# Performance work log

Hardware: AMD Instinct MI355X
Metric: run time of the kernel (lower is better)

Reference implementation:

```python
import jax, jax.numpy as jnp
import numpy as np
import math

NUM_PARAM = 9
STRIDE = 1
BN_EPS = 1e-5


def _make_p_n(N):
    # matches LDConv._get_p_n: irregular kernel offset grid of N points
    base = round(math.sqrt(N))
    rows = N // base
    mod = N % base
    gx, gy = np.meshgrid(np.arange(rows), np.arange(base), indexing='ij')
    px, py = gx.ravel(), gy.ravel()
    if mod > 0:
        mx, my = np.meshgrid(np.arange(rows, rows + 1), np.arange(mod), indexing='ij')
        px = np.concatenate([px, mx.ravel()])
        py = np.concatenate([py, my.ravel()])
    return jnp.asarray(np.concatenate([px, py]), jnp.float32).reshape(1, 2 * N, 1, 1)


def _conv2d_same(x, w, stride, pad):
    return jax.lax.conv_general_dilated(
        x, w, (stride, stride), [(pad, pad), (pad, pad)],
        dimension_numbers=('NCHW', 'OIHW', 'NCHW'))


def _gather(xf, q, W, N):
    # xf: (b,c,H*W); q: (b,h,w,2N) int indices -> (b,c,h,w,N)
    idx = q[..., :N] * W + q[..., N:]
    return jax.vmap(lambda xb, ib: xb[:, ib])(xf, idx)


def setup_inputs() -> dict:
    key = jax.random.key(0)
    ks = jax.random.split(key, 3)
    B, C, H, W = 8, 128, 64, 64
    outc = 256
    x = jax.random.normal(ks[0], (B, C, H, W), jnp.float32)
    # p_conv init: uniform(-1e-4, 1e-4) weights, zero bias (per the torch module)
    p_conv_w = jax.random.uniform(ks[1], (2 * NUM_PARAM, C, 3, 3), jnp.float32, -1e-4, 1e-4)
    p_conv_b = jnp.zeros((2 * NUM_PARAM,), jnp.float32)
    conv_w = jax.random.normal(ks[2], (outc, C, NUM_PARAM, 1), jnp.float32) / math.sqrt(C * NUM_PARAM)
    bn_gamma = jnp.ones((outc,), jnp.float32)
    bn_beta = jnp.zeros((outc,), jnp.float32)
    bn_mean = jnp.zeros((outc,), jnp.float32)
    bn_var = jnp.ones((outc,), jnp.float32)
    return dict(x=x, p_conv_w=p_conv_w, p_conv_b=p_conv_b, conv_w=conv_w,
                bn_gamma=bn_gamma, bn_beta=bn_beta, bn_mean=bn_mean, bn_var=bn_var)


def reference(x, p_conv_w, p_conv_b, conv_w, bn_gamma, bn_beta, bn_mean, bn_var):
    N = NUM_PARAM
    B, C, H, W = x.shape
    offset = _conv2d_same(x, p_conv_w, STRIDE, 1) + p_conv_b[None, :, None, None]  # (b,2N,h,w)
    h, w = offset.shape[2], offset.shape[3]
    gx, gy = jnp.meshgrid(jnp.arange(0, h * STRIDE, STRIDE),
                          jnp.arange(0, w * STRIDE, STRIDE), indexing='ij')
    p_0 = jnp.concatenate([jnp.broadcast_to(gx, (1, N, h, w)),
                           jnp.broadcast_to(gy, (1, N, h, w))], axis=1).astype(x.dtype)
    p = (p_0 + _make_p_n(N) + offset).transpose(0, 2, 3, 1)  # (b,h,w,2N)

    q_lt = jnp.floor(jax.lax.stop_gradient(p))
    q_rb = q_lt + 1
    clampi = lambda q: jnp.concatenate([jnp.clip(q[..., :N], 0, H - 1),
                                        jnp.clip(q[..., N:], 0, W - 1)], -1).astype(jnp.int32)
    q_lt = clampi(q_lt)
    q_rb = clampi(q_rb)
    q_lb = jnp.concatenate([q_lt[..., :N], q_rb[..., N:]], -1)
    q_rt = jnp.concatenate([q_rb[..., :N], q_lt[..., N:]], -1)
    p = jnp.concatenate([jnp.clip(p[..., :N], 0, H - 1),
                         jnp.clip(p[..., N:], 0, W - 1)], -1)
    f = lambda q: q.astype(p.dtype)
    g_lt = (1 + (f(q_lt[..., :N]) - p[..., :N])) * (1 + (f(q_lt[..., N:]) - p[..., N:]))
    g_rb = (1 - (f(q_rb[..., :N]) - p[..., :N])) * (1 - (f(q_rb[..., N:]) - p[..., N:]))
    g_lb = (1 + (f(q_lb[..., :N]) - p[..., :N])) * (1 - (f(q_lb[..., N:]) - p[..., N:]))
    g_rt = (1 - (f(q_rt[..., :N]) - p[..., :N])) * (1 + (f(q_rt[..., N:]) - p[..., N:]))

    xf = x.reshape(B, C, H * W)
    x_off = (g_lt[:, None] * _gather(xf, q_lt, W, N)
             + g_rb[:, None] * _gather(xf, q_rb, W, N)
             + g_lb[:, None] * _gather(xf, q_lb, W, N)
             + g_rt[:, None] * _gather(xf, q_rt, W, N))  # (b,c,h,w,N)
    # rearrange 'b c h w n -> b c (h n) w'
    x_off = x_off.transpose(0, 1, 2, 4, 3).reshape(B, C, h * N, w)

    y = jax.lax.conv_general_dilated(x_off, conv_w, (N, 1), 'VALID',
                                     dimension_numbers=('NCHW', 'OIHW', 'NCHW'))
    scale = (bn_gamma / jnp.sqrt(bn_var + BN_EPS))[None, :, None, None]
    y = (y - bn_mean[None, :, None, None]) * scale + bn_beta[None, :, None, None]
    return y * jax.nn.sigmoid(y)  # SiLU
```

## Files before the change

### kernel.cpp

```cpp
#include <hip/hip_runtime.h>
#include <hip/hip_bf16.h>
#include <cstdint>

#define B_   8
#define C_   128
#define H_   64
#define W_   64
#define NPT  9
#define OC   256
#define K_   (C_*NPT)
#define HW   (H_*W_)
#define XTPB 557568

typedef __attribute__((ext_vector_type(8))) short short8;
typedef __attribute__((ext_vector_type(4))) float f32x4;
typedef __attribute__((ext_vector_type(4))) unsigned int u32x4;

static __device__ __forceinline__ unsigned short f2bf(float f) {
    union { float f; unsigned u; } a; a.f = f;
    unsigned r = a.u + 0x7fffu + ((a.u >> 16) & 1u);
    return (unsigned short)(r >> 16);
}
static __device__ __forceinline__ float bf2f(unsigned short u) {
    union { unsigned u; float f; } a; a.u = ((unsigned)u) << 16;
    return a.f;
}

__global__ __launch_bounds__(256) void k_transpose2(const float* __restrict__ x,
                                                    unsigned short* __restrict__ xh,
                                                    unsigned short* __restrict__ xl) {
    __shared__ float sp[128][65];
    int b = blockIdx.x >> 6, i = blockIdx.x & 63;
    int t = threadIdx.x;
    const float* xb = x + (size_t)b * C_ * HW + i * 64;
#pragma unroll
    for (int it = 0; it < 8; ++it) {
        int q = it * 256 + t;
        int c = q >> 4, j4 = q & 15;
        *(f32x4*)&sp[c][j4 * 4] = *(const f32x4*)(xb + (size_t)c * HW + j4 * 4);
    }
    __syncthreads();
    size_t obase = (size_t)b * XTPB + ((size_t)(i + 1) * 66 + 1) * 128;
#pragma unroll
    for (int it = 0; it < 4; ++it) {
        int q = it * 256 + t;
        int j = q >> 4, cg = q & 15;
        u32x4 ph, pl;
#pragma unroll
        for (int p2 = 0; p2 < 4; ++p2) {
            float a = sp[cg * 8 + p2 * 2][j];
            float bb = sp[cg * 8 + p2 * 2 + 1][j];
            unsigned short ah = f2bf(a), bh = f2bf(bb);
            unsigned short al = f2bf(a - bf2f(ah)), bl = f2bf(bb - bf2f(bh));
            ph[p2] = (uint32_t)ah | ((uint32_t)bh << 16);
            pl[p2] = (uint32_t)al | ((uint32_t)bl << 16);
        }
        *(u32x4*)(xh + obase + (size_t)j * 128 + cg * 8) = ph;
        *(u32x4*)(xl + obase + (size_t)j * 128 + cg * 8) = pl;
    }
    size_t rowb = (size_t)b * XTPB + (size_t)(i + 1) * 66 * 128;
    if (t < 128) {
        xh[rowb + t] = 0; xl[rowb + t] = 0;
    } else {
        xh[rowb + 65 * 128 + (t - 128)] = 0; xl[rowb + 65 * 128 + (t - 128)] = 0;
    }
    if (i == 0) {
        size_t r0b = (size_t)b * XTPB;
        for (int e = t; e < 8448; e += 256) { xh[r0b + e] = 0; xl[r0b + e] = 0; }
    }
    if (i == 63) {
        size_t r65 = (size_t)b * XTPB + (size_t)65 * 66 * 128;
        for (int e = t; e < 8448; e += 256) { xh[r65 + e] = 0; xl[r65 + e] = 0; }
    }
}

__global__ __launch_bounds__(256) void k_prepow2(const float* __restrict__ pw,
                                                 unsigned short* __restrict__ wh,
                                                 unsigned short* __restrict__ wl) {
    int idx = blockIdx.x * 256 + threadIdx.x;
    int o = idx / 1152, kp = idx - o * 1152;
    int tp = kp >> 7, c = kp & 127;
    float v = (o < 18) ? pw[o * K_ + c * 9 + tp] : 0.f;
    unsigned short hi = f2bf(v);
    unsigned short lo = f2bf(v - bf2f(hi));
    int db = (o * 2304 + tp * 256 + ((c * 2) ^ ((o & 7) << 4))) >> 1;
    wh[db] = hi;
    wl[db] = lo;
}

__global__ __launch_bounds__(256) void k_offgemm2(const unsigned short* __restrict__ xh,
                                                  const unsigned short* __restrict__ xl,
                                                  const unsigned short* __restrict__ wh,
                                                  const unsigned short* __restrict__ wl,
                                                  const float* __restrict__ pb,
                                                  float* __restrict__ off) {
    __shared__ __align__(16) char smem[81920];
    int bid = blockIdx.x;
    int wg = (bid & 7) * 32 + (bid >> 3);
    int b = wg >> 5;
    int i0 = (wg & 31) * 2;
    int tid = threadIdx.x;
    int wv = tid >> 6, lane = tid & 63;
    int lrow = lane & 15, lg = lane >> 4;
    const char* xhb = (const char*)(xh + (size_t)b * XTPB);
    const char* xlb = (const char*)(xl + (size_t)b * XTPB);
    const char* whb = (const char*)wh;
    const char* wlb = (const char*)wl;

    f32x4 zero = {0.f, 0.f, 0.f, 0.f};
    f32x4 acc[2][2];
#pragma unroll
    for (int m = 0; m < 2; ++m)
#pragma unroll
        for (int n = 0; n < 2; ++n) acc[m][n] = zero;

    for (int tpt = 0; tpt < 9; ++tpt) {
        int dh = tpt / 3 - 1, dw = tpt % 3 - 1;
#pragma unroll
        for (int q = 0; q < 8; ++q) {
            int ch = q * 256 + tid;
            int row = ch >> 4, slot = ch & 15;
            int ri = i0 + (row >> 6) + dh + 1;
            int ci = (row & 63) + dw + 1;
            int src = (ri * 66 + ci) * 256 + ((slot * 16) ^ ((row & 7) << 4));
            __builtin_amdgcn_global_load_lds(
                (const __attribute__((address_space(1))) uint32_t*)(xhb + src),
                (__attribute__((address_space(3))) uint32_t*)(smem + ch * 16), 16, 0, 0);
            __builtin_amdgcn_global_load_lds(
                (const __attribute__((address_space(1))) uint32_t*)(xlb + src),
                (__attribute__((address_space(3))) uint32_t*)(smem + 32768 + ch * 16), 16, 0, 0);
        }
#pragma unroll
        for (int q = 0; q < 2; ++q) {
            int ch = q * 256 + tid;
            int row = ch >> 4, slot = ch & 15;
            int src = row * 2304 + tpt * 256 + slot * 16;
            __builtin_amdgcn_global_load_lds(
                (const __attribute__((address_space(1))) uint32_t*)(whb + src),
                (__attribute__((address_space(3))) uint32_t*)(smem + 65536 + ch * 16), 16, 0, 0);
            __builtin_amdgcn_global_load_lds(
                (const __attribute__((address_space(1))) uint32_t*)(wlb + src),
                (__attribute__((address_space(3))) uint32_t*)(smem + 73728 + ch * 16), 16, 0, 0);
        }
        __syncthreads();
#pragma unroll
        for (int ks = 0; ks < 4; ++ks) {
            short8 ah[2], al[2], bh[2], bl[2];
#pragma unroll
            for (int m = 0; m < 2; ++m) {
                int row = wv * 32 + m * 16 + lrow;
                int byt = (ks * 64 + lg * 16) ^ ((row & 7) << 4);
                ah[m] = *(const short8*)(smem + row * 256 + byt);
                al[m] = *(const short8*)(smem + 32768 + row * 256 + byt);
            }
#pragma unroll
            for (int n = 0; n < 2; ++n) {
                int row = n * 16 + lrow;
                int byt = (ks * 64 + lg * 16) ^ ((row & 7) << 4);
                bh[n] = *(const short8*)(smem + 65536 + row * 256 + byt);
                bl[n] = *(const short8*)(smem + 73728 + row * 256 + byt);
            }
#pragma unroll
            for (int m = 0; m < 2; ++m)
#pragma unroll
                for (int n = 0; n < 2; ++n) {
                    acc[m][n] = __builtin_amdgcn_mfma_f32_16x16x32_bf16(ah[m], bh[n], acc[m][n], 0, 0, 0);
                    acc[m][n] = __builtin_amdgcn_mfma_f32_16x16x32_bf16(ah[m], bl[n], acc[m][n], 0, 0, 0);
                    acc[m][n] = __builtin_amdgcn_mfma_f32_16x16x32_bf16(al[m], bh[n], acc[m][n], 0, 0, 0);
                    acc[m][n] = __builtin_amdgcn_mfma_f32_16x16x32_bf16(al[m], bl[n], acc[m][n], 0, 0, 0);
                }
        }
        __syncthreads();
    }
#pragma unroll
    for (int n = 0; n < 2; ++n) {
        int oc = n * 16 + lrow;
        if (oc < 18) {
            float bs = pb[oc];
#pragma unroll
            for (int m = 0; m < 2; ++m) {
#pragma unroll
                for (int r = 0; r < 4; ++r) {
                    int px = wv * 32 + m * 16 + lg * 4 + r;
                    int ii = i0 + (px >> 6), jj = px & 63;
                    off[(((size_t)b * 18 + oc) * H_ + ii) * W_ + jj] = acc[m][n][r] + bs;
                }
            }
        }
    }
}

__global__ __launch_bounds__(256) void k_prepw(const float* __restrict__ cw,
                                               const float* __restrict__ gam,
                                               const float* __restrict__ bet,
                                               const float* __restrict__ mu,
                                               const float* __restrict__ var,
                                               unsigned short* __restrict__ wbf,
                                               float* __restrict__ bias) {
    int idx = blockIdx.x * 256 + threadIdx.x;
    int oc = idx / K_;
    int r = idx - oc * K_;
    int n = r >> 7;
    int c = r & 127;
    float sc = gam[oc] * rsqrtf(var[oc] + 1e-5f);
    wbf[idx] = f2bf(cw[oc * K_ + c * NPT + n] * sc);
    if (blockIdx.x == 0 && threadIdx.x < OC) {
        int o = threadIdx.x;
        float s = gam[o] * rsqrtf(var[o] + 1e-5f);
        bias[o] = bet[o] - mu[o] * s;
    }
}

__global__ __launch_bounds__(512, 4) void k_fused(const unsigned short* __restrict__ xh,
                                                  const float* __restrict__ off,
                                                  const unsigned short* __restrict__ wbf,
                                                  const float* __restrict__ bias,
                                                  float* __restrict__ out) {
    __shared__ __align__(16) char smem[70144];
    int bid = blockIdx.x;
    int wg = (bid & 7) * 64 + (bid >> 3);
    int b = wg >> 6;
    int i = wg & 63;
    int tid = threadIdx.x;
    int wv = tid >> 6, lane = tid & 63, j = lane;
    int lrow = lane & 15, lg = lane >> 4;
    const unsigned short* xTb = xh + (size_t)b * XTPB;
    const char* Bb = (const char*)wbf;
    float* soff = (float*)(smem + 65536);

    auto stageB = [&](int buf, int hs) {
        char* base = smem + 16384 + buf * 16384;
#pragma unroll
        for (int q = 0; q < 2; ++q) {
            int ch = q * 512 + tid;
            int row = ch >> 2, slot = ch & 3;
            int src = row * 2304 + hs * 64 + ((slot ^ (row & 3)) * 16);
            __builtin_amdgcn_global_load_lds(
                (const __attribute__((address_space(1))) uint32_t*)(Bb + src),
                (__attribute__((address_space(3))) uint32_t*)(base + ch * 16), 16, 0, 0);
        }
    };

    short8 tp0, tp1, tp2, tp3;
    float w00, w11, w01, w10;
    auto gather_issue = [&](int kt) {
        int n = kt >> 1;
        int c8 = (kt & 1) * 8 + wv;
        float ox = soff[n * 64 + j];
        float oy = soff[(n + 9) * 64 + j];
        float pxf = (float)(i + n / 3) + ox;
        float pyf = (float)(j + n % 3) + oy;
        float fx = floorf(pxf), fy = floorf(pyf);
        int r0 = max(0, min(63, (int)fx));
        int r1 = max(0, min(63, (int)fx + 1));
        int c0 = max(0, min(63, (int)fy));
        int c1 = max(0, min(63, (int)fy + 1));
        float pxc = fminf(fmaxf(pxf, 0.f), 63.f);
        float pyc = fminf(fmaxf(pyf, 0.f), 63.f);
        float ax = 1.f + ((float)r0 - pxc);
        float bx = 1.f - ((float)r1 - pxc);
        float ay = 1.f + ((float)c0 - pyc);
        float by = 1.f - ((float)c1 - pyc);
        w00 = ax * ay; w11 = bx * by; w01 = ax * by; w10 = bx * ay;
        const unsigned short* g = xTb + c8 * 8;
        int rb0 = (r0 + 1) * 66, rb1 = (r1 + 1) * 66;
        tp0 = *(const short8*)(g + (size_t)(rb0 + c0 + 1) * C_);
        tp1 = *(const short8*)(g + (size_t)(rb1 + c1 + 1) * C_);
        tp2 = *(const short8*)(g + (size_t)(rb0 + c1 + 1) * C_);
        tp3 = *(const short8*)(g + (size_t)(rb1 + c0 + 1) * C_);
    };
    auto bilinear_write = [&](int kt) {
        u32x4 pk;
#pragma unroll
        for (int p2 = 0; p2 < 4; ++p2) {
            unsigned short rr[2];
#pragma unroll
            for (int e = 0; e < 2; ++e) {
                int ei = p2 * 2 + e;
                float v = w00 * bf2f((unsigned short)tp0[ei])
                        + w11 * bf2f((unsigned short)tp1[ei])
                        + w01 * bf2f((unsigned short)tp2[ei])
                        + w10 * bf2f((unsigned short)tp3[ei]);
                rr[e] = f2bf(v);
            }
            pk[p2] = (uint32_t)rr[0] | ((uint32_t)rr[1] << 16);
        }
        *(u32x4*)(smem + (kt & 1) * 8192 + wv * 1024 + j * 16) = pk;
    };

    f32x4 zero = {0.f, 0.f, 0.f, 0.f};
    f32x4 acc[4][2];
#pragma unroll
    for (int m = 0; m < 4; ++m)
#pragma unroll
        for (int n = 0; n < 2; ++n) acc[m][n] = zero;

    auto compute_half = [&](int abuf, int bbuf, int h) {
        const char* sa = smem + abuf * 8192;
        const char* sb = smem + 16384 + bbuf * 16384;
        short8 afr[4], bfr[2];
#pragma unroll
        for (int m = 0; m < 4; ++m)
            afr[m] = *(const short8*)(sa + (h * 4 + lg) * 1024 + (m * 16 + lrow) * 16);
#pragma unroll
        for (int n = 0; n < 2; ++n) {
            int row = wv * 32 + n * 16 + lrow;
            bfr[n] = *(const short8*)(sb + row * 64 + ((lg ^ (row & 3)) * 16));
        }
#pragma unroll
        for (int m = 0; m < 4; ++m)
#pragma unroll
            for (int n = 0; n < 2; ++n)
                acc[m][n] = __builtin_amdgcn_mfma_f32_16x16x32_bf16(afr[m], bfr[n], acc[m][n], 0, 0, 0);
    };

    for (int e = tid; e < 1152; e += 512) {
        int plane = e >> 6, jj = e & 63;
        soff[e] = off[(((size_t)b * 18 + plane) * H_ + i) * W_ + jj];
    }
    stageB(0, 0);
    stageB(1, 1);
    __syncthreads();
    gather_issue(0);
    bilinear_write(0);
    stageB(2, 2);
    __syncthreads();

#pragma unroll 6
    for (int kt = 0; kt < 18; ++kt) {
        const int hs0 = 2 * kt;
        if (hs0 + 2 < 36) stageB((hs0 + 2) % 3, hs0 + 2);
        if (kt < 17) gather_issue(kt + 1);
        compute_half(kt & 1, hs0 % 3, 0);
        __syncthreads();
        if (hs0 + 3 < 36) stageB((hs0 + 3) % 3, hs0 + 3);
        if (kt < 17) bilinear_write(kt + 1);
        compute_half(kt & 1, (hs0 + 1) % 3, 1);
        __syncthreads();
    }

#pragma unroll
    for (int n = 0; n < 2; ++n) {
        int oc = wv * 32 + n * 16 + lrow;
        float bs = bias[oc];
#pragma unroll
        for (int m = 0; m < 4; ++m) {
#pragma unroll
            for (int r = 0; r < 4; ++r) {
                int px = m * 16 + lg * 4 + r;
                float v = acc[m][n][r] + bs;
                float sv = v / (1.f + __expf(-v));
                out[((size_t)b * OC + oc) * HW + i * 64 + px] = sv;
            }
        }
    }
}

extern "C" void kernel_launch(void* const* d_in, const int* in_sizes, int n_in,
                              void* d_out, int out_size, void* d_ws, size_t ws_size,
                              hipStream_t stream) {
    const float* x   = (const float*)d_in[0];
    const float* pw  = (const float*)d_in[1];
    const float* pb  = (const float*)d_in[2];
    const float* cw  = (const float*)d_in[3];
    const float* gam = (const float*)d_in[4];
    const float* bet = (const float*)d_in[5];
    const float* mu  = (const float*)d_in[6];
    const float* var = (const float*)d_in[7];
    float* out = (float*)d_out;

    char* ws = (char*)d_ws;
    float* off           = (float*)ws;
    unsigned short* wbf  = (unsigned short*)(ws + 2359296);
    float* bias          = (float*)(ws + 2949120);
    unsigned short* whi  = (unsigned short*)(ws + 2950144);
    unsigned short* wlo  = (unsigned short*)(ws + 3023872);
    unsigned short* xh   = (unsigned short*)(ws + 3097600);
    unsigned short* xl   = (unsigned short*)(ws + 12018688);

    hipLaunchKernelGGL(k_transpose2, dim3(512),  dim3(256), 0, stream, x, xh, xl);
    hipLaunchKernelGGL(k_prepow2,    dim3(144),  dim3(256), 0, stream, pw, whi, wlo);
    hipLaunchKernelGGL(k_prepw,      dim3(1152), dim3(256), 0, stream, cw, gam, bet, mu, var, wbf, bias);
    hipLaunchKernelGGL(k_offgemm2,   dim3(256),  dim3(256), 0, stream, xh, xl, whi, wlo, pb, off);
    hipLaunchKernelGGL(k_fused,      dim3(512),  dim3(512), 0, stream, xh, off, wbf, bias, out);
}
```

Before: 97.61 us.

## Process two output rows per workgroup to halve weight staging traffic

Each workgroup of the fused gather+GEMM kernel now covers two image rows (128 pixels) instead of one. The grid is halved, per-wave accumulators double to 8x2 MFMA tiles, and each thread gathers two channel groups per step. This halves the number of times the bf16 weight matrix is streamed from global memory into LDS. In exchange, LDS use grows to about 89 KB, launch bounds drop to 2 blocks per CU, and there are only 256 workgroups, which reduces occupancy and latency hiding for the gathers.

```diff
diff --git a/kernel.cpp b/kernel.cpp
--- a/kernel.cpp
+++ b/kernel.cpp
@@ -211,25 +211,29 @@
     }
 }
 
-__global__ __launch_bounds__(512, 4) void k_fused(const unsigned short* __restrict__ xh,
+__global__ __launch_bounds__(512, 2) void k_fused(const unsigned short* __restrict__ xh,
                                                   const float* __restrict__ off,
                                                   const unsigned short* __restrict__ wbf,
                                                   const float* __restrict__ bias,
                                                   float* __restrict__ out) {
-    __shared__ __align__(16) char smem[70144];
+    __shared__ __align__(16) char smem[91136];
     int bid = blockIdx.x;
-    int wg = (bid & 7) * 64 + (bid >> 3);
-    int b = wg >> 6;
-    int i = wg & 63;
+    int wg = (bid & 7) * 32 + (bid >> 3);
+    int b = wg >> 5;
+    int i0 = (wg & 31) * 2;
     int tid = threadIdx.x;
-    int wv = tid >> 6, lane = tid & 63, j = lane;
+    int wv = tid >> 6, lane = tid & 63;
     int lrow = lane & 15, lg = lane >> 4;
+    int gpx = tid & 127;
+    int gs0 = tid >> 7;
+    int gii = i0 + (gpx >> 6);
+    int gjj = gpx & 63;
     const unsigned short* xTb = xh + (size_t)b * XTPB;
     const char* Bb = (const char*)wbf;
-    float* soff = (float*)(smem + 65536);
+    float* soff = (float*)(smem + 81920);
 
     auto stageB = [&](int buf, int hs) {
-        char* base = smem + 16384 + buf * 16384;
+        char* base = smem + 32768 + buf * 16384;
 #pragma unroll
         for (int q = 0; q < 2; ++q) {
             int ch = q * 512 + tid;
@@ -241,15 +245,16 @@
         }
     };
 
-    short8 tp0, tp1, tp2, tp3;
+    short8 tpa0, tpa1, tpa2, tpa3, tpb0, tpb1, tpb2, tpb3;
     float w00, w11, w01, w10;
     auto gather_issue = [&](int kt) {
         int n = kt >> 1;
-        int c8 = (kt & 1) * 8 + wv;
-        float ox = soff[n * 64 + j];
-        float oy = soff[(n + 9) * 64 + j];
-        float pxf = (float)(i + n / 3) + ox;
-        float pyf = (float)(j + n % 3) + oy;
+        int c8a = (kt & 1) * 8 + gs0;
+        int c8b = c8a + 4;
+        float ox = soff[(gpx >> 6) * 1152 + n * 64 + gjj];
+        float oy = soff[(gpx >> 6) * 1152 + (n + 9) * 64 + gjj];
+        float pxf = (float)(gii + n / 3) + ox;
+        float pyf = (float)(gjj + n % 3) + oy;
         float fx = floorf(pxf), fy = floorf(pyf);
         int r0 = max(0, min(63, (int)fx));
         int r1 = max(0, min(63, (int)fx + 1));
@@ -262,14 +267,19 @@
         float ay = 1.f + ((float)c0 - pyc);
         float by = 1.f - ((float)c1 - pyc);
         w00 = ax * ay; w11 = bx * by; w01 = ax * by; w10 = bx * ay;
-        const unsigned short* g = xTb + c8 * 8;
         int rb0 = (r0 + 1) * 66, rb1 = (r1 + 1) * 66;
-        tp0 = *(const short8*)(g + (size_t)(rb0 + c0 + 1) * C_);
-        tp1 = *(const short8*)(g + (size_t)(rb1 + c1 + 1) * C_);
-        tp2 = *(const short8*)(g + (size_t)(rb0 + c1 + 1) * C_);
-        tp3 = *(const short8*)(g + (size_t)(rb1 + c0 + 1) * C_);
+        const unsigned short* ga = xTb + c8a * 8;
+        const unsigned short* gb = xTb + c8b * 8;
+        tpa0 = *(const short8*)(ga + (size_t)(rb0 + c0 + 1) * C_);
+        tpa1 = *(const short8*)(ga + (size_t)(rb1 + c1 + 1) * C_);
+        tpa2 = *(const short8*)(ga + (size_t)(rb0 + c1 + 1) * C_);
+        tpa3 = *(const short8*)(ga + (size_t)(rb1 + c0 + 1) * C_);
+        tpb0 = *(const short8*)(gb + (size_t)(rb0 + c0 + 1) * C_);
+        tpb1 = *(const short8*)(gb + (size_t)(rb1 + c1 + 1) * C_);
+        tpb2 = *(const short8*)(gb + (size_t)(rb0 + c1 + 1) * C_);
+        tpb3 = *(const short8*)(gb + (size_t)(rb1 + c0 + 1) * C_);
     };
-    auto bilinear_write = [&](int kt) {
+    auto bilin1 = [&](const short8& t0, const short8& t1, const short8& t2, const short8& t3) {
         u32x4 pk;
 #pragma unroll
         for (int p2 = 0; p2 < 4; ++p2) {
@@ -277,46 +287,53 @@
 #pragma unroll
             for (int e = 0; e < 2; ++e) {
                 int ei = p2 * 2 + e;
-                float v = w00 * bf2f((unsigned short)tp0[ei])
-                        + w11 * bf2f((unsigned short)tp1[ei])
-                        + w01 * bf2f((unsigned short)tp2[ei])
-                        + w10 * bf2f((unsigned short)tp3[ei]);
+                float v = w00 * bf2f((unsigned short)t0[ei])
+                        + w11 * bf2f((unsigned short)t1[ei])
+                        + w01 * bf2f((unsigned short)t2[ei])
+                        + w10 * bf2f((unsigned short)t3[ei]);
                 rr[e] = f2bf(v);
             }
             pk[p2] = (uint32_t)rr[0] | ((uint32_t)rr[1] << 16);
         }
-        *(u32x4*)(smem + (kt & 1) * 8192 + wv * 1024 + j * 16) = pk;
+        return pk;
     };
+    auto bilinear_write = [&](int kt) {
+        u32x4 pa = bilin1(tpa0, tpa1, tpa2, tpa3);
+        u32x4 pb2 = bilin1(tpb0, tpb1, tpb2, tpb3);
+        char* abuf = smem + (kt & 1) * 16384;
+        *(u32x4*)(abuf + gs0 * 2048 + gpx * 16) = pa;
+        *(u32x4*)(abuf + (gs0 + 4) * 2048 + gpx * 16) = pb2;
+    };
 
     f32x4 zero = {0.f, 0.f, 0.f, 0.f};
-    f32x4 acc[4][2];
-#pragma unroll
-    for (int m = 0; m < 4; ++m)
+    f32x4 acc[8][2];
+#pragma unroll
+    for (int m = 0; m < 8; ++m)
 #pragma unroll
         for (int n = 0; n < 2; ++n) acc[m][n] = zero;
 
     auto compute_half = [&](int abuf, int bbuf, int h) {
-        const char* sa = smem + abuf * 8192;
-        const char* sb = smem + 16384 + bbuf * 16384;
-        short8 afr[4], bfr[2];
-#pragma unroll
-        for (int m = 0; m < 4; ++m)
-            afr[m] = *(const short8*)(sa + (h * 4 + lg) * 1024 + (m * 16 + lrow) * 16);
+        const char* sa = smem + abuf * 16384;
+        const char* sb = smem + 32768 + bbuf * 16384;
+        short8 bfr[2];
 #pragma unroll
         for (int n = 0; n < 2; ++n) {
             int row = wv * 32 + n * 16 + lrow;
             bfr[n] = *(const short8*)(sb + row * 64 + ((lg ^ (row & 3)) * 16));
         }
 #pragma unroll
-        for (int m = 0; m < 4; ++m)
+        for (int m = 0; m < 8; ++m) {
+            short8 afr = *(const short8*)(sa + (h * 4 + lg) * 2048 + (m * 16 + lrow) * 16);
 #pragma unroll
             for (int n = 0; n < 2; ++n)
-                acc[m][n] = __builtin_amdgcn_mfma_f32_16x16x32_bf16(afr[m], bfr[n], acc[m][n], 0, 0, 0);
+                acc[m][n] = __builtin_amdgcn_mfma_f32_16x16x32_bf16(afr, bfr[n], acc[m][n], 0, 0, 0);
+        }
     };
 
-    for (int e = tid; e < 1152; e += 512) {
-        int plane = e >> 6, jj = e & 63;
-        soff[e] = off[(((size_t)b * 18 + plane) * H_ + i) * W_ + jj];
+    for (int e = tid; e < 2304; e += 512) {
+        int r = e / 1152, rem = e - r * 1152;
+        int plane = rem >> 6, jj = rem & 63;
+        soff[e] = off[(((size_t)b * 18 + plane) * H_ + (i0 + r)) * W_ + jj];
     }
     stageB(0, 0);
     stageB(1, 1);
@@ -344,13 +361,13 @@
         int oc = wv * 32 + n * 16 + lrow;
         float bs = bias[oc];
 #pragma unroll
-        for (int m = 0; m < 4; ++m) {
+        for (int m = 0; m < 8; ++m) {
 #pragma unroll
             for (int r = 0; r < 4; ++r) {
                 int px = m * 16 + lg * 4 + r;
                 float v = acc[m][n][r] + bs;
                 float sv = v / (1.f + __expf(-v));
-                out[((size_t)b * OC + oc) * HW + i * 64 + px] = sv;
+                out[((size_t)b * OC + oc) * HW + (i0 + (px >> 6)) * W_ + (px & 63)] = sv;
             }
         }
     }
@@ -382,5 +399,5 @@
     hipLaunchKernelGGL(k_prepow2,    dim3(144),  dim3(256), 0, stream, pw, whi, wlo);
     hipLaunchKernelGGL(k_prepw,      dim3(1152), dim3(256), 0, stream, cw, gam, bet, mu, var, wbf, bias);
     hipLaunchKernelGGL(k_offgemm2,   dim3(256),  dim3(256), 0, stream, xh, xl, whi, wlo, pb, off);
-    hipLaunchKernelGGL(k_fused,      dim3(512),  dim3(512), 0, stream, xh, off, wbf, bias, out);
-}
+    hipLaunchKernelGGL(k_fused,      dim3(256),  dim3(512), 0, stream, xh, off, wbf, bias, out);
+}
```

New measurement: 100.1 us. 1.03x slower.
